# Optimization experiments

Hardware: AMD Instinct MI355X
Metric: run time of the kernel (lower is better)

Reference implementation:

```python
import jax, jax.numpy as jnp
import numpy as np

IN_F = 4096
OUT_F = 4096
RANK = 8
ALPHA = 8
SCALE = ALPHA / RANK


def setup_inputs() -> dict:
    key = jax.random.key(0)
    kx, kw, kb, ka = jax.random.split(key, 4)
    x = jax.random.normal(kx, (4, 4096, IN_F), dtype=jnp.float32)
    # base frozen linear params (torch Linear default init style, any values ok)
    W = jax.random.normal(kw, (OUT_F, IN_F), dtype=jnp.float32) * (1.0 / np.sqrt(IN_F))
    b = jax.random.normal(kb, (OUT_F,), dtype=jnp.float32) * 0.01
    # lora_A: kaiming_uniform_(a=sqrt(5)) -> U(-bound, bound), bound = sqrt(6/((1+5)*in_f)) = 1/sqrt(in_f)
    bound = 1.0 / np.sqrt(IN_F)
    lora_A = jax.random.uniform(ka, (RANK, IN_F), dtype=jnp.float32, minval=-bound, maxval=bound)
    # lora_B initialized to zeros per module; use small random values so the LoRA path is exercised
    lora_B = jax.random.normal(jax.random.fold_in(key, 7), (OUT_F, RANK), dtype=jnp.float32) * 0.02
    return {"x": x, "W": W, "b": b, "lora_A": lora_A, "lora_B": lora_B}


def reference(x, W, b, lora_A, lora_B):
    # base: x @ W.T + b  [B,S,out_f]
    base = jnp.einsum("bsi,oi->bso", x, W) + b
    # low-rank path: (x @ A.T) @ B.T * scale
    xa = jnp.einsum("bsi,ri->bsr", x, lora_A)  # [B,S,r]
    lora = jnp.einsum("bsr,or->bso", xa, lora_B)
    return base + lora * SCALE
```

## Files before the change

kernel.cpp:

```cpp
#include <hip/hip_runtime.h>
#include <cstdint>

#define K_IN   4096
#define N_OUT  4096
#define M_ROWS 16384
#define RANK   8
#define LSCALE 1.0f
#define NT     64
#define ROWB   8192
#define AHALF  1048576

typedef __attribute__((ext_vector_type(8))) short  short8;
typedef __attribute__((ext_vector_type(4))) float  floatx4;

__device__ __forceinline__ unsigned short f2bf(float f) {
  uint32_t u = __float_as_uint(f);
  u += 0x7FFFu + ((u >> 16) & 1u);
  return (unsigned short)(u >> 16);
}

__global__ __launch_bounds__(256) void fold_w_kernel(
    const float* __restrict__ W, const float* __restrict__ lA,
    const float* __restrict__ lB, unsigned short* __restrict__ Weff) {
  int idx = blockIdx.x * 256 + threadIdx.x;
  int o = idx >> 10;
  int k = (idx & 1023) << 2;
  float4 w = *reinterpret_cast<const float4*>(W + (size_t)o * K_IN + k);
#pragma unroll
  for (int r = 0; r < RANK; ++r) {
    float s = LSCALE * lB[o * RANK + r];
    float4 a = *reinterpret_cast<const float4*>(lA + r * K_IN + k);
    w.x += s * a.x; w.y += s * a.y; w.z += s * a.z; w.w += s * a.w;
  }
  ushort4 p;
  p.x = f2bf(w.x); p.y = f2bf(w.y); p.z = f2bf(w.z); p.w = f2bf(w.w);
  *reinterpret_cast<ushort4*>(Weff + (size_t)o * K_IN + k) = p;
}

__global__ __launch_bounds__(256) void cvt_x_kernel(
    const float* __restrict__ x, unsigned short* __restrict__ xb) {
  size_t i = ((size_t)blockIdx.x * 256 + threadIdx.x) * 8;
  float4 a = *reinterpret_cast<const float4*>(x + i);
  float4 c = *reinterpret_cast<const float4*>(x + i + 4);
  uint4 v;
  v.x = (uint32_t)f2bf(a.x) | ((uint32_t)f2bf(a.y) << 16);
  v.y = (uint32_t)f2bf(a.z) | ((uint32_t)f2bf(a.w) << 16);
  v.z = (uint32_t)f2bf(c.x) | ((uint32_t)f2bf(c.y) << 16);
  v.w = (uint32_t)f2bf(c.z) | ((uint32_t)f2bf(c.w) << 16);
  *reinterpret_cast<uint4*>(xb + i) = v;
}

__device__ __forceinline__ void gload_lds16(const void* g, void* l) {
  __builtin_amdgcn_global_load_lds(
      (const __attribute__((address_space(1))) void*)g,
      (__attribute__((address_space(3))) void*)l, 16, 0, 0);
}

#define BAR() do { asm volatile("" ::: "memory");                         \
    __builtin_amdgcn_s_barrier();                                         \
    asm volatile("" ::: "memory"); } while (0)

#define DSR(DST, ADDR, IMM)                                               \
  asm volatile("ds_read_b128 %0, %1 offset:%2"                            \
               : "=v"(DST) : "v"(ADDR), "i"(IMM))
#define LGKM(N) do {                                                      \
    asm volatile("s_waitcnt lgkmcnt(" #N ")" ::: "memory");               \
    __builtin_amdgcn_sched_barrier(0); } while (0)
#define VMW(N) do {                                                       \
    asm volatile("s_waitcnt vmcnt(" #N ")" ::: "memory");                 \
    __builtin_amdgcn_sched_barrier(0); } while (0)

__global__ __launch_bounds__(512, 2) void gemm256_kernel(
    const unsigned short* __restrict__ Xb, const unsigned short* __restrict__ Wb,
    const float* __restrict__ bias, float* __restrict__ out) {
  __shared__ alignas(16) char lds[2 * 65536];

  const int tid  = threadIdx.x;
  const int wave = tid >> 6, lane = tid & 63;
  const int wr = wave >> 2, wc = wave & 3;
  const int l15 = lane & 15, sq = lane >> 4;

  int bx  = blockIdx.x;
  int sbx = (bx & 7) * 128 + (bx >> 3);
  const int mt = sbx >> 4;
  const int nt = sbx & 15;

  const int rstg = tid >> 3;
  const int cbst = (((tid & 7) ^ ((tid >> 3) & 7)) << 4);
  const char* aBase = (const char*)Xb + (size_t)(mt * 256 + rstg) * ROWB + cbst;
  const char* bBase = (const char*)Wb + (size_t)(nt * 256 + rstg) * ROWB + cbst;

#define STAGE_TH(TH, HH) do {                                             \
    const char* src_ = ((HH) < 2 ? aBase + (size_t)(HH) * AHALF           \
                                 : bBase + (size_t)((HH) - 2) * AHALF)    \
                       + (TH) * 128;                                      \
    char* dst_ = lds + ((TH) & 1) * 65536 + (HH) * 16384 + tid * 16;      \
    gload_lds16(src_, dst_);                                              \
    gload_lds16(src_ + (size_t)64 * ROWB, dst_ + 8192);                   \
  } while (0)

  const unsigned ldsb = (unsigned)(unsigned long long)
      (__attribute__((address_space(3))) char*)lds;
  const unsigned X = (unsigned)((l15 & 7) << 4);
  const unsigned aRow = ldsb + wr * 16384 + l15 * 128;
  const unsigned bRow = ldsb + (2 + (wc >> 1)) * 16384 + (wc & 1) * 8192
                        + l15 * 128;
  unsigned aCur0 = aRow + ((0u  + sq * 16) ^ X);
  unsigned aCur1 = aRow + ((64u + sq * 16) ^ X);
  unsigned bCur0 = bRow + ((0u  + sq * 16) ^ X);
  unsigned bCur1 = bRow + ((64u + sq * 16) ^ X);

#define LOAD_A(DST, MQ) do {                                              \
    _Pragma("unroll")                                                     \
    for (int fi = 0; fi < 4; ++fi)                                        \
      DSR(DST[fi],     aCur0, (MQ) * 8192 + fi * 2048);                   \
    _Pragma("unroll")                                                     \
    for (int fi = 0; fi < 4; ++fi)                                        \
      DSR(DST[4 + fi], aCur1, (MQ) * 8192 + fi * 2048);                   \
  } while (0)
#define LOAD_B4(DST, NQ) do {                                             \
    DSR(DST[0], bCur0, (NQ) * 4096);                                      \
    DSR(DST[1], bCur0, (NQ) * 4096 + 2048);                               \
    DSR(DST[2], bCur1, (NQ) * 4096);                                      \
    DSR(DST[3], bCur1, (NQ) * 4096 + 2048);                               \
  } while (0)
#define MFMA_Q(MQ, NQ, AF, BF) do {                                       \
    __builtin_amdgcn_s_setprio(1);                                        \
    _Pragma("unroll")                                                     \
    for (int ks = 0; ks < 2; ++ks)                                        \
      _Pragma("unroll")                                                   \
      for (int fi = 0; fi < 4; ++fi)                                      \
        _Pragma("unroll")                                                 \
        for (int fj = 0; fj < 2; ++fj)                                    \
          acc[(MQ) * 4 + fi][(NQ) * 2 + fj] =                             \
              __builtin_amdgcn_mfma_f32_16x16x32_bf16(                    \
                  AF[ks * 4 + fi], BF[ks * 2 + fj],                       \
                  acc[(MQ) * 4 + fi][(NQ) * 2 + fj], 0, 0, 0);            \
    __builtin_amdgcn_s_setprio(0); } while (0)

  floatx4 acc[8][4];
#pragma unroll
  for (int i = 0; i < 8; ++i)
#pragma unroll
    for (int j = 0; j < 4; ++j)
      acc[i][j] = (floatx4){0.f, 0.f, 0.f, 0.f};

  STAGE_TH(0, 0); STAGE_TH(0, 1); STAGE_TH(0, 2); STAGE_TH(0, 3);
  STAGE_TH(1, 0); STAGE_TH(1, 1); STAGE_TH(1, 2);
  VMW(6);
  BAR();

  short8 afA[8], afB[8], bfC[4], bfD[4];
  LOAD_A(afA, 0);
  LOAD_B4(bfC, 0);

  for (int t = 0; t < NT; ++t) {
    LOAD_B4(bfD, 1);
    LOAD_A(afB, 1);
    if (t <= NT - 2) STAGE_TH(t + 1, 3);
    LGKM(12);
    MFMA_Q(0, 0, afA, bfC);
    BAR();

    if (t <= NT - 3) STAGE_TH(t + 2, 0);
    LGKM(8);
    MFMA_Q(0, 1, afA, bfD);
    BAR();

    if (t <= NT - 3) STAGE_TH(t + 2, 1);
    LGKM(0);
    MFMA_Q(1, 0, afB, bfC);
    if (t <= NT - 3)      VMW(4);
    else if (t == NT - 2) VMW(0);
    BAR();

    if (t <= NT - 2) {
      aCur0 ^= 65536u; aCur1 ^= 65536u; bCur0 ^= 65536u; bCur1 ^= 65536u;
      LOAD_A(afA, 0);
      LOAD_B4(bfC, 0);
    }
    if (t <= NT - 3) STAGE_TH(t + 2, 2);
    __builtin_amdgcn_sched_barrier(0);
    MFMA_Q(1, 1, afB, bfD);
    BAR();
  }
#undef STAGE_TH
#undef LOAD_A
#undef LOAD_B4
#undef MFMA_Q

  const int row0 = mt * 256 + wr * 128 + sq * 4;
  const int col0 = nt * 256 + wc * 64 + l15;
#pragma unroll
  for (int j = 0; j < 4; ++j) {
    int col = col0 + j * 16;
    float bv = bias[col];
#pragma unroll
    for (int i = 0; i < 8; ++i) {
      int rowb = row0 + i * 16;
#pragma unroll
      for (int rr = 0; rr < 4; ++rr)
        out[(size_t)(rowb + rr) * N_OUT + col] = acc[i][j][rr] + bv;
    }
  }
}

__global__ __launch_bounds__(256) void fallback_kernel(
    const float* __restrict__ x, const float* __restrict__ W,
    const float* __restrict__ bias, const float* __restrict__ lA,
    const float* __restrict__ lB, float* __restrict__ out) {
  __shared__ float Xs[64][17];
  __shared__ float Ws[64][17];
  int tid = threadIdx.x;
  int tx = tid & 15, ty = tid >> 4;
  int bm = blockIdx.y * 64, bn = blockIdx.x * 64;
  float acc[4][4] = {};
  for (int k0 = 0; k0 < K_IN; k0 += 16) {
#pragma unroll
    for (int q = 0; q < 4; ++q) {
      int flat = q * 256 + tid;
      int r = flat >> 4, c = flat & 15;
      Xs[r][c] = x[(size_t)(bm + r) * K_IN + k0 + c];
      float w = W[(size_t)(bn + r) * K_IN + k0 + c];
#pragma unroll
      for (int rr = 0; rr < RANK; ++rr)
        w += LSCALE * lB[(bn + r) * RANK + rr] * lA[rr * K_IN + k0 + c];
      Ws[r][c] = w;
    }
    __syncthreads();
#pragma unroll
    for (int kk = 0; kk < 16; ++kk) {
      float av[4], bv[4];
#pragma unroll
      for (int i = 0; i < 4; ++i) av[i] = Xs[ty * 4 + i][kk];
#pragma unroll
      for (int j = 0; j < 4; ++j) bv[j] = Ws[tx * 4 + j][kk];
#pragma unroll
      for (int i = 0; i < 4; ++i)
#pragma unroll
        for (int j = 0; j < 4; ++j) acc[i][j] += av[i] * bv[j];
    }
    __syncthreads();
  }
#pragma unroll
  for (int i = 0; i < 4; ++i)
#pragma unroll
    for (int j = 0; j < 4; ++j)
      out[(size_t)(bm + ty * 4 + i) * N_OUT + bn + tx * 4 + j] =
          acc[i][j] + bias[bn + tx * 4 + j];
}

extern "C" void kernel_launch(void* const* d_in, const int* in_sizes, int n_in,
                              void* d_out, int out_size, void* d_ws, size_t ws_size,
                              hipStream_t stream) {
  const float* x  = (const float*)d_in[0];
  const float* W  = (const float*)d_in[1];
  const float* b  = (const float*)d_in[2];
  const float* lA = (const float*)d_in[3];
  const float* lB = (const float*)d_in[4];
  float* out = (float*)d_out;

  const size_t weff_bytes = (size_t)N_OUT * K_IN * 2;
  const size_t xb_bytes   = (size_t)M_ROWS * K_IN * 2;

  if (ws_size >= weff_bytes + xb_bytes) {
    unsigned short* Weff = (unsigned short*)d_ws;
    unsigned short* Xb   = (unsigned short*)((char*)d_ws + weff_bytes);
    fold_w_kernel<<<(int)(((size_t)N_OUT * K_IN / 4) / 256), 256, 0, stream>>>(W, lA, lB, Weff);
    cvt_x_kernel<<<(int)(((size_t)M_ROWS * K_IN / 8) / 256), 256, 0, stream>>>(x, Xb);
    gemm256_kernel<<<(M_ROWS / 256) * (N_OUT / 256), 512, 0, stream>>>(Xb, Weff, b, out);
  } else {
    dim3 grid(N_OUT / 64, M_ROWS / 64);
    fallback_kernel<<<grid, 256, 0, stream>>>(x, W, b, lA, lB, out);
  }
}
```

Measured before the change: 572.6 us.

## Switch GEMM to 32x32x16 bf16 MFMA with matching LDS fragment layout

Result: slower. 670.8 us (+17.1%).

```diff
diff --git a/kernel.cpp b/kernel.cpp
--- a/kernel.cpp
+++ b/kernel.cpp
@@ -8,10 +8,10 @@
 #define LSCALE 1.0f
 #define NT     64
 #define ROWB   8192
-#define AHALF  1048576
-
-typedef __attribute__((ext_vector_type(8))) short  short8;
-typedef __attribute__((ext_vector_type(4))) float  floatx4;
+
+typedef __attribute__((ext_vector_type(8)))  short short8;
+typedef __attribute__((ext_vector_type(4)))  float floatx4;
+typedef __attribute__((ext_vector_type(16))) float floatx16;
 
 __device__ __forceinline__ unsigned short f2bf(float f) {
   uint32_t u = __float_as_uint(f);
@@ -78,72 +78,70 @@
   const int tid  = threadIdx.x;
   const int wave = tid >> 6, lane = tid & 63;
   const int wr = wave >> 2, wc = wave & 3;
-  const int l15 = lane & 15, sq = lane >> 4;
 
   int bx  = blockIdx.x;
   int sbx = (bx & 7) * 128 + (bx >> 3);
   const int mt = sbx >> 4;
   const int nt = sbx & 15;
 
-  const int rstg = tid >> 3;
-  const int cbst = (((tid & 7) ^ ((tid >> 3) & 7)) << 4);
-  const char* aBase = (const char*)Xb + (size_t)(mt * 256 + rstg) * ROWB + cbst;
-  const char* bBase = (const char*)Wb + (size_t)(nt * 256 + rstg) * ROWB + cbst;
+  const char* aSrc = (const char*)Xb
+      + (size_t)(mt * 256 + (wave >> 2) * 32 + (lane & 31)) * ROWB
+      + (wave & 3) * 32 + (lane >> 5) * 16;
+  const char* bSrc = (const char*)Wb
+      + (size_t)(nt * 256 + (wave >> 2) * 32 + (lane & 31)) * ROWB
+      + (wave & 3) * 32 + (lane >> 5) * 16;
 
 #define STAGE_TH(TH, HH) do {                                             \
-    const char* src_ = ((HH) < 2 ? aBase + (size_t)(HH) * AHALF           \
-                                 : bBase + (size_t)((HH) - 2) * AHALF)    \
-                       + (TH) * 128;                                      \
-    char* dst_ = lds + ((TH) & 1) * 65536 + (HH) * 16384 + tid * 16;      \
-    gload_lds16(src_, dst_);                                              \
-    gload_lds16(src_ + (size_t)64 * ROWB, dst_ + 8192);                   \
-  } while (0)
+    char* bufb_ = lds + ((TH) & 1) * 65536;                               \
+    if ((HH) < 2) {                                                       \
+      const char* s_ = aSrc + (TH) * 128 + (size_t)((HH) * 2) * 524288;   \
+      char* d_ = bufb_ + (HH) * 16384 + tid * 16;                         \
+      gload_lds16(s_, d_);                                                \
+      gload_lds16(s_ + 524288, d_ + 8192);                                \
+    } else {                                                              \
+      const char* s_ = bSrc + (TH) * 128 + (size_t)(((HH) - 2) * 2) * 524288; \
+      char* d_ = bufb_ + 32768 + ((HH) - 2) * 16384 + tid * 16;           \
+      gload_lds16(s_, d_);                                                \
+      gload_lds16(s_ + 524288, d_ + 8192);                                \
+    } } while (0)
 
   const unsigned ldsb = (unsigned)(unsigned long long)
       (__attribute__((address_space(3))) char*)lds;
-  const unsigned X = (unsigned)((l15 & 7) << 4);
-  const unsigned aRow = ldsb + wr * 16384 + l15 * 128;
-  const unsigned bRow = ldsb + (2 + (wc >> 1)) * 16384 + (wc & 1) * 8192
-                        + l15 * 128;
-  unsigned aCur0 = aRow + ((0u  + sq * 16) ^ X);
-  unsigned aCur1 = aRow + ((64u + sq * 16) ^ X);
-  unsigned bCur0 = bRow + ((0u  + sq * 16) ^ X);
-  unsigned bCur1 = bRow + ((64u + sq * 16) ^ X);
-
-#define LOAD_A(DST, MQ) do {                                              \
+  unsigned aCur = ldsb + wr * 16384 + lane * 16;
+  unsigned bCur = ldsb + 32768 + wc * 8192 + lane * 16;
+
+#define LOAD_A(DST, MH) do {                                              \
     _Pragma("unroll")                                                     \
-    for (int fi = 0; fi < 4; ++fi)                                        \
-      DSR(DST[fi],     aCur0, (MQ) * 8192 + fi * 2048);                   \
-    _Pragma("unroll")                                                     \
-    for (int fi = 0; fi < 4; ++fi)                                        \
-      DSR(DST[4 + fi], aCur1, (MQ) * 8192 + fi * 2048);                   \
+    for (int m2 = 0; m2 < 2; ++m2)                                        \
+      _Pragma("unroll")                                                   \
+      for (int ks = 0; ks < 4; ++ks)                                      \
+        DSR(DST[m2 * 4 + ks], aCur,                                       \
+            (MH) * 8192 + m2 * 4096 + ks * 1024);                         \
   } while (0)
 #define LOAD_B4(DST, NQ) do {                                             \
-    DSR(DST[0], bCur0, (NQ) * 4096);                                      \
-    DSR(DST[1], bCur0, (NQ) * 4096 + 2048);                               \
-    DSR(DST[2], bCur1, (NQ) * 4096);                                      \
-    DSR(DST[3], bCur1, (NQ) * 4096 + 2048);                               \
+    _Pragma("unroll")                                                     \
+    for (int ks = 0; ks < 4; ++ks)                                        \
+      DSR(DST[ks], bCur, (NQ) * 4096 + ks * 1024);                        \
   } while (0)
 #define MFMA_Q(MQ, NQ, AF, BF) do {                                       \
     __builtin_amdgcn_s_setprio(1);                                        \
     _Pragma("unroll")                                                     \
-    for (int ks = 0; ks < 2; ++ks)                                        \
+    for (int m2 = 0; m2 < 2; ++m2)                                        \
       _Pragma("unroll")                                                   \
-      for (int fi = 0; fi < 4; ++fi)                                      \
-        _Pragma("unroll")                                                 \
-        for (int fj = 0; fj < 2; ++fj)                                    \
-          acc[(MQ) * 4 + fi][(NQ) * 2 + fj] =                             \
-              __builtin_amdgcn_mfma_f32_16x16x32_bf16(                    \
-                  AF[ks * 4 + fi], BF[ks * 2 + fj],                       \
-                  acc[(MQ) * 4 + fi][(NQ) * 2 + fj], 0, 0, 0);            \
+      for (int ks = 0; ks < 4; ++ks)                                      \
+        acc[(MQ) * 2 + m2][NQ] =                                          \
+            __builtin_amdgcn_mfma_f32_32x32x16_bf16(                      \
+                AF[m2 * 4 + ks], BF[ks], acc[(MQ) * 2 + m2][NQ], 0, 0, 0);\
     __builtin_amdgcn_s_setprio(0); } while (0)
 
-  floatx4 acc[8][4];
-#pragma unroll
-  for (int i = 0; i < 8; ++i)
-#pragma unroll
-    for (int j = 0; j < 4; ++j)
-      acc[i][j] = (floatx4){0.f, 0.f, 0.f, 0.f};
+  floatx16 acc[4][2];
+#pragma unroll
+  for (int i = 0; i < 4; ++i)
+#pragma unroll
+    for (int j = 0; j < 2; ++j)
+#pragma unroll
+      for (int r = 0; r < 16; ++r)
+        acc[i][j][r] = 0.f;
 
   STAGE_TH(0, 0); STAGE_TH(0, 1); STAGE_TH(0, 2); STAGE_TH(0, 3);
   STAGE_TH(1, 0); STAGE_TH(1, 1); STAGE_TH(1, 2);
@@ -175,7 +173,7 @@
     BAR();
 
     if (t <= NT - 2) {
-      aCur0 ^= 65536u; aCur1 ^= 65536u; bCur0 ^= 65536u; bCur1 ^= 65536u;
+      aCur ^= 65536u; bCur ^= 65536u;
       LOAD_A(afA, 0);
       LOAD_B4(bfC, 0);
     }
@@ -189,18 +187,19 @@
 #undef LOAD_B4
 #undef MFMA_Q
 
-  const int row0 = mt * 256 + wr * 128 + sq * 4;
-  const int col0 = nt * 256 + wc * 64 + l15;
-#pragma unroll
-  for (int j = 0; j < 4; ++j) {
-    int col = col0 + j * 16;
+  const int rowb0 = mt * 256 + wr * 128 + ((lane >> 5) << 2);
+  const int colL  = nt * 256 + wc * 64 + (lane & 31);
+#pragma unroll
+  for (int nf = 0; nf < 2; ++nf) {
+    int col = colL + nf * 32;
     float bv = bias[col];
 #pragma unroll
-    for (int i = 0; i < 8; ++i) {
-      int rowb = row0 + i * 16;
-#pragma unroll
-      for (int rr = 0; rr < 4; ++rr)
-        out[(size_t)(rowb + rr) * N_OUT + col] = acc[i][j][rr] + bv;
+    for (int mf = 0; mf < 4; ++mf) {
+#pragma unroll
+      for (int r = 0; r < 16; ++r) {
+        int row = rowb0 + mf * 32 + (r & 3) + ((r >> 2) << 3);
+        out[(size_t)row * N_OUT + col] = acc[mf][nf][r] + bv;
+      }
     }
   }
 }
```
